# Optimization experiments

Measured on AMD Instinct MI355X. Metric: run time of the kernel, lower is better.

Reference implementation:

```python
import jax, jax.numpy as jnp
import numpy as np
from jax import lax

B, L, D = 8, 2048, 512


def _mlp(x, w1, w2):
    # MemoryMLP: x + gelu(x @ w1) @ w2  (exact gelu, matching F.gelu default)
    return x + jax.nn.gelu(x @ w1, approximate=False) @ w2


def _l2norm(t):
    # F.normalize(p=2, dim=-1, eps=1e-12)
    n = jnp.linalg.norm(t, axis=-1, keepdims=True)
    return t / jnp.maximum(n, 1e-12)


def setup_inputs() -> dict:
    key = jax.random.key(0)
    ks = jax.random.split(key, 12)
    s = 0.02
    return {
        "x": jax.random.normal(ks[0], (B, L, D), jnp.float32),
        "conv_w": jax.random.normal(ks[1], (D, 1, 4), jnp.float32) * s,  # depthwise, (out, in/groups, k)
        "conv_b": jax.random.normal(ks[2], (D,), jnp.float32) * s,
        "q_w": jax.random.normal(ks[3], (D, D), jnp.float32) * s,  # Linear weight (out, in)
        "mem_w1": jax.random.normal(ks[4], (D, D), jnp.float32) * s,
        "mem_w2": jax.random.normal(ks[5], (D, D), jnp.float32) * s,
        "eta_w1": jax.random.normal(ks[6], (D, D), jnp.float32) * s,
        "eta_w2": jax.random.normal(ks[7], (D, D), jnp.float32) * s,
        "alpha_w1": jax.random.normal(ks[8], (D, D), jnp.float32) * s,
        "alpha_w2": jax.random.normal(ks[9], (D, D), jnp.float32) * s,
    }


def _forward(x, conv_w, conv_b, q_w, mem_w1, mem_w2, eta_w1, eta_w2, alpha_w1, alpha_w2):
    # causal depthwise conv: Conv1d(k=4, padding=3, groups=D) then slice [:L] == left-pad 3
    xc = lax.conv_general_dilated(
        jnp.transpose(x, (0, 2, 1)),  # (B, D, L)
        conv_w,                        # (D, 1, 4)
        window_strides=(1,),
        padding=[(3, 0)],
        feature_group_count=D,
        dimension_numbers=("NCH", "OIH", "NCH"),
    ) + conv_b[None, :, None]
    xc = jnp.transpose(xc, (0, 2, 1))  # (B, L, D)

    # time-invariant branches (m_k/m_v weights are never updated; kt/vt/hat_v do not
    # affect the output, so they are elided). q, eta, alpha use fixed weights -> vectorize.
    q = _l2norm(xc @ q_w.T)                                   # (B, L, D)
    eta_mean = jax.nn.sigmoid(_mlp(xc, eta_w1, eta_w2)).mean(axis=(0, 2))      # (L,)
    alpha_mean = jax.nn.sigmoid(_mlp(xc, alpha_w1, alpha_w2)).mean(axis=(0, 2))  # (L,)

    def step(carry, inp):
        w1, w2 = carry
        q_t, a_t, e_t = inp  # (B, D), (), ()
        o_t = _mlp(q_t, w1, w2)  # output uses pre-update memory
        new_w1 = w1 * a_t - e_t * 0.01
        new_w2 = w2 * a_t - e_t * 0.01
        return (new_w1, new_w2), o_t

    qs = jnp.transpose(q, (1, 0, 2))  # (L, B, D)
    (_, _), outs = lax.scan(step, (mem_w1, mem_w2), (qs, alpha_mean, eta_mean))
    return jnp.transpose(outs, (1, 0, 2))  # (B, L, D)


def reference(x, conv_w, conv_b, q_w, mem_w1, mem_w2, eta_w1, eta_w2, alpha_w1, alpha_w2):
    return _forward(x, conv_w, conv_b, q_w, mem_w1, mem_w2, eta_w1, eta_w2, alpha_w1, alpha_w2)
```

## Files before the change

kernel.cpp:

```cpp
#include <hip/hip_runtime.h>
#include <math.h>

constexpr int Bn = 8, Ln = 2048, Dn = 512;
constexpr int Mn = Bn * Ln;
constexpr int CONV_BLOCKS = Mn * Dn / 4 / 256;

typedef __bf16 bf16x8 __attribute__((ext_vector_type(8)));
typedef __bf16 bf16x4v __attribute__((ext_vector_type(4)));
typedef float f32x4 __attribute__((ext_vector_type(4)));

__device__ __forceinline__ float gelu_exact(float x) {
    return 0.5f * x * (1.0f + erff(x * 0.7071067811865475f));
}
__device__ __forceinline__ float sigmoid_fast(float x) {
    return __builtin_amdgcn_rcpf(1.0f + __expf(-x));
}

__global__ __launch_bounds__(256) void prep_kernel(
    const float* __restrict__ x, const float* __restrict__ w,
    const float* __restrict__ bias, __bf16* __restrict__ xcb,
    const float* __restrict__ ew1, const float* __restrict__ aw1,
    const float* __restrict__ ew2, const float* __restrict__ aw2,
    const float* __restrict__ mw1, const float* __restrict__ mw2,
    const float* __restrict__ qw,
    __bf16* __restrict__ Wall, __bf16* __restrict__ W2t,
    __bf16* __restrict__ m1t, __bf16* __restrict__ m2t) {
    __shared__ float tile[64][65];
    if (blockIdx.x < CONV_BLOCKS) {
        int idx = blockIdx.x * 256 + threadIdx.x;
        int g = idx & 127;
        int bl = idx >> 7;
        int l = bl & (Ln - 1);
        int d = g * 4;
        float a[4];
        float4 b4 = *(const float4*)&bias[d];
        a[0] = b4.x; a[1] = b4.y; a[2] = b4.z; a[3] = b4.w;
        float wv[16];
        *(float4*)&wv[0]  = *(const float4*)&w[d * 4];
        *(float4*)&wv[4]  = *(const float4*)&w[d * 4 + 4];
        *(float4*)&wv[8]  = *(const float4*)&w[d * 4 + 8];
        *(float4*)&wv[12] = *(const float4*)&w[d * 4 + 12];
#pragma unroll
        for (int k = 0; k < 4; ++k) {
            int ll = l - 3 + k;
            if (ll >= 0) {
                float4 xv = *(const float4*)&x[(size_t)(bl - 3 + k) * Dn + d];
                a[0] += xv.x * wv[0 * 4 + k];
                a[1] += xv.y * wv[1 * 4 + k];
                a[2] += xv.z * wv[2 * 4 + k];
                a[3] += xv.w * wv[3 * 4 + k];
            }
        }
        bf16x4v o = { (__bf16)a[0], (__bf16)a[1], (__bf16)a[2], (__bf16)a[3] };
        *(bf16x4v*)&xcb[(size_t)bl * Dn + d] = o;
        return;
    }
    int bid = blockIdx.x - CONV_BLOCKS;
    int z = bid >> 6;
    int t = bid & 63;
    int r0 = (t >> 3) * 64, c0 = (t & 7) * 64;
    const float* src;
    __bf16* dst;
    int trans = 1;
    switch (z) {
        case 0: src = ew1; dst = Wall; break;
        case 1: src = aw1; dst = Wall + 512 * 512; break;
        case 2: src = ew2; dst = W2t; break;
        case 3: src = aw2; dst = W2t + 512 * 512; break;
        case 4: src = mw1; dst = m1t; break;
        case 5: src = mw2; dst = m2t; break;
        default: src = qw; dst = Wall + 1024 * 512; trans = 0; break;
    }
    if (!trans) {
        for (int i = threadIdx.x; i < 4096; i += 256) {
            int r = i >> 6, c = i & 63;
            dst[(size_t)(r0 + r) * 512 + c0 + c] = (__bf16)src[(size_t)(r0 + r) * 512 + c0 + c];
        }
        return;
    }
    for (int i = threadIdx.x; i < 4096; i += 256) {
        int r = i >> 6, c = i & 63;
        tile[r][c] = src[(size_t)(r0 + r) * 512 + c0 + c];
    }
    __syncthreads();
    for (int i = threadIdx.x; i < 4096; i += 256) {
        int r = i >> 6, c = i & 63;
        dst[(size_t)(c0 + r) * 512 + r0 + c] = (__bf16)tile[c][r];
    }
}

template <int OP, int BM>
__global__ __launch_bounds__(256, 2) void gemm_mfma(
    const __bf16* __restrict__ A, int lda, int Az,
    const __bf16* __restrict__ Bt, int Bz,
    void* __restrict__ C0, void* __restrict__ C1,
    const __bf16* __restrict__ auxb,
    const float* __restrict__ Pv, const float* __restrict__ Qv,
    const float* __restrict__ SSv, const float* __restrict__ RSv,
    float* __restrict__ red0, float* __restrict__ red1, float* __restrict__ red2) {
    constexpr int MI = BM / 32;
    constexpr int AISS = BM / 64;
    __shared__ __align__(16) __bf16 Asl[BM * 32];
    __shared__ __align__(16) __bf16 Bsl[128 * 32];
    const int tid = threadIdx.x;
    const int lane = tid & 63, wv = tid >> 6;
    const int wm = wv & 1, wn = wv >> 1;
    const int fr = lane & 15, fq = lane >> 4;
    const int z = blockIdx.z;
    A += (size_t)z * Az;
    Bt += (size_t)z * Bz;
    const __bf16* Ab = A + (size_t)blockIdx.y * BM * lda;
    const __bf16* Bb = Bt + (size_t)blockIdx.x * 128 * 512;
    float* redp = (OP == 1) ? red0 + (size_t)z * Ln : red0;

    f32x4 acc[MI][4] = {};

    for (int k0 = 0; k0 < 512; k0 += 32) {
#pragma unroll
        for (int i = 0; i < AISS; ++i) {
            int c = tid + i * 256;
            int r = c >> 2, co = (c & 3) * 8;
            __builtin_amdgcn_global_load_lds(
                (const __attribute__((address_space(1))) void*)(Ab + (size_t)r * lda + k0 + co),
                (__attribute__((address_space(3))) void*)(Asl + c * 8), 16, 0, 0);
        }
#pragma unroll
        for (int i = 0; i < 2; ++i) {
            int c = tid + i * 256;
            int r = c >> 2, co = (c & 3) * 8;
            __builtin_amdgcn_global_load_lds(
                (const __attribute__((address_space(1))) void*)(Bb + (size_t)r * 512 + k0 + co),
                (__attribute__((address_space(3))) void*)(Bsl + c * 8), 16, 0, 0);
        }
        __syncthreads();
        bf16x8 af[MI], bfr[4];
#pragma unroll
        for (int mi = 0; mi < MI; ++mi)
            af[mi] = *(const bf16x8*)&Asl[(wm * (BM / 2) + mi * 16 + fr) * 32 + fq * 8];
#pragma unroll
        for (int ni = 0; ni < 4; ++ni)
            bfr[ni] = *(const bf16x8*)&Bsl[(wn * 64 + ni * 16 + fr) * 32 + fq * 8];
#pragma unroll
        for (int mi = 0; mi < MI; ++mi)
#pragma unroll
            for (int ni = 0; ni < 4; ++ni)
                acc[mi][ni] = __builtin_amdgcn_mfma_f32_16x16x32_bf16(af[mi], bfr[ni], acc[mi][ni], 0, 0, 0);
        __syncthreads();
    }

    const int row_base = blockIdx.y * BM + wm * (BM / 2);
    const int col_base = blockIdx.x * 128 + wn * 64;
    const bool qpath = (OP == 0) && (blockIdx.x >= 8);
#pragma unroll
    for (int mi = 0; mi < MI; ++mi) {
#pragma unroll
        for (int r = 0; r < 4; ++r) {
            int row = row_base + mi * 16 + fq * 4 + r;
            float p = 0.f, qs = 0.f, rs = 0.f, inv = 1.f;
            if (OP >= 3) {
                int t = row & (Ln - 1);
                p = Pv[t]; qs = Qv[t];
                rs = RSv[row];
                inv = 1.0f / fmaxf(sqrtf(SSv[row]), 1e-12f);
            }
            float s1 = 0.f, s2 = 0.f;
#pragma unroll
            for (int ni = 0; ni < 4; ++ni) {
                int col = col_base + ni * 16 + fr;
                float v = acc[mi][ni][r];
                if (OP == 0) {
                    if (!qpath) {
                        v = gelu_exact(v);
                        ((__bf16*)C0)[(size_t)row * 1024 + col] = (__bf16)v;
                    } else {
                        ((__bf16*)C1)[(size_t)row * 512 + col - 1024] = (__bf16)v;
                        s1 += v; s2 += v * v;
                    }
                } else if (OP == 1) {
                    v = sigmoid_fast((float)auxb[(size_t)row * 512 + col] + v);
                    s1 += v;
                } else if (OP == 3) {
                    v = gelu_exact(inv * (p * v + qs * rs));
                    ((__bf16*)C0)[(size_t)row * 512 + col] = (__bf16)v;
                    s1 += v;
                } else if (OP == 4) {
                    float qn = (float)auxb[(size_t)row * 512 + col] * inv;
                    ((float*)C0)[(size_t)row * 512 + col] = qn + p * v + qs * rs;
                }
            }
            if (OP == 1 || OP == 3 || (OP == 0 && qpath)) {
                s1 += __shfl_xor(s1, 1, 64);
                s1 += __shfl_xor(s1, 2, 64);
                s1 += __shfl_xor(s1, 4, 64);
                s1 += __shfl_xor(s1, 8, 64);
                if (OP == 0) {
                    s2 += __shfl_xor(s2, 1, 64);
                    s2 += __shfl_xor(s2, 2, 64);
                    s2 += __shfl_xor(s2, 4, 64);
                    s2 += __shfl_xor(s2, 8, 64);
                }
                if (fr == 0) {
                    if (OP == 1) atomicAdd(&redp[row & (Ln - 1)], s1 * (1.0f / 4096.0f));
                    else if (OP == 3) atomicAdd(&red0[row], s1);
                    else { atomicAdd(&red1[row], s2); atomicAdd(&red2[row], s1); }
                }
            }
        }
    }
}

__global__ __launch_bounds__(256) void scan_kernel(const float* __restrict__ a,
                                                   const float* __restrict__ e,
                                                   float* __restrict__ P,
                                                   float* __restrict__ Q) {
    int tid = threadIdx.x;
    int base = tid * 8;
    float la[8], le[8], Aloc[8], Bloc[8];
#pragma unroll
    for (int j = 0; j < 8; ++j) { la[j] = a[base + j]; le[j] = e[base + j]; }
    float Ac = 1.f, Bc = 0.f;
#pragma unroll
    for (int j = 0; j < 8; ++j) {
        Aloc[j] = Ac; Bloc[j] = Bc;
        Bc = Bc * la[j] - 0.01f * le[j];
        Ac *= la[j];
    }
    float Aw = Ac, Bw = Bc;
#pragma unroll
    for (int off = 1; off < 64; off <<= 1) {
        float Ap = __shfl_up(Aw, off, 64);
        float Bp = __shfl_up(Bw, off, 64);
        if ((tid & 63) >= off) { Bw = Aw * Bp + Bw; Aw = Aw * Ap; }
    }
    __shared__ float wA[4], wB[4];
    if ((tid & 63) == 63) { wA[tid >> 6] = Aw; wB[tid >> 6] = Bw; }
    __syncthreads();
    float Apre = 1.f, Bpre = 0.f;
    for (int w = 0; w < (tid >> 6); ++w) { Bpre = wA[w] * Bpre + wB[w]; Apre = wA[w] * Apre; }
    float Ax = __shfl_up(Aw, 1, 64), Bx = __shfl_up(Bw, 1, 64);
    if ((tid & 63) == 0) { Ax = 1.f; Bx = 0.f; }
    float At = Ax * Apre, Bt2 = Ax * Bpre + Bx;
#pragma unroll
    for (int j = 0; j < 8; ++j) {
        P[base + j] = Aloc[j] * At;
        Q[base + j] = Aloc[j] * Bt2 + Bloc[j];
    }
}

extern "C" void kernel_launch(void* const* d_in, const int* in_sizes, int n_in,
                              void* d_out, int out_size, void* d_ws, size_t ws_size,
                              hipStream_t stream) {
    const float* x        = (const float*)d_in[0];
    const float* conv_w   = (const float*)d_in[1];
    const float* conv_b   = (const float*)d_in[2];
    const float* q_w      = (const float*)d_in[3];
    const float* mem_w1   = (const float*)d_in[4];
    const float* mem_w2   = (const float*)d_in[5];
    const float* eta_w1   = (const float*)d_in[6];
    const float* eta_w2   = (const float*)d_in[7];
    const float* alpha_w1 = (const float*)d_in[8];
    const float* alpha_w2 = (const float*)d_in[9];
    float* out = (float*)d_out;

    char* w = (char*)d_ws;
    __bf16* xcb  = (__bf16*)w;    w += (size_t)Mn * Dn * 2;
    __bf16* H    = (__bf16*)w;    w += (size_t)Mn * 1024 * 2;
    __bf16* qb   = (__bf16*)w;    w += (size_t)Mn * Dn * 2;
    __bf16* G    = (__bf16*)w;    w += (size_t)Mn * Dn * 2;
    __bf16* Wall = (__bf16*)w;    w += (size_t)1536 * 512 * 2;
    __bf16* W2t  = (__bf16*)w;    w += (size_t)2 * 512 * 512 * 2;
    __bf16* m1t  = (__bf16*)w;    w += (size_t)512 * 512 * 2;
    __bf16* m2t  = (__bf16*)w;    w += (size_t)512 * 512 * 2;
    float* Rv      = (float*)w;   w += (size_t)Mn * 4;
    float* MeanAcc = (float*)w;   w += (size_t)2 * Ln * 4;
    float* SS      = (float*)w;   w += (size_t)Mn * 4;
    float* RS      = (float*)w;   w += (size_t)Mn * 4;
    float* Pv = (float*)w;        w += Ln * 4;
    float* Qv = (float*)w;        w += Ln * 4;

    hipMemsetAsync(Rv, 0, (size_t)(Mn + 2 * Ln + Mn + Mn) * 4, stream);

    prep_kernel<<<CONV_BLOCKS + 448, 256, 0, stream>>>(
        x, conv_w, conv_b, xcb, eta_w1, alpha_w1, eta_w2, alpha_w2,
        mem_w1, mem_w2, q_w, Wall, W2t, m1t, m2t);
    gemm_mfma<0, 128><<<dim3(12, 128), 256, 0, stream>>>(
        xcb, 512, 0, Wall, 0, H, qb, nullptr,
        nullptr, nullptr, nullptr, nullptr, nullptr, SS, RS);
    gemm_mfma<1, 128><<<dim3(4, 128, 2), 256, 0, stream>>>(
        H, 1024, 512, W2t, 512 * 512, nullptr, nullptr, xcb,
        nullptr, nullptr, nullptr, nullptr, MeanAcc, nullptr, nullptr);
    scan_kernel<<<1, 256, 0, stream>>>(MeanAcc + Ln, MeanAcc, Pv, Qv);
    gemm_mfma<3, 64><<<dim3(4, 256), 256, 0, stream>>>(
        qb, 512, 0, m1t, 0, G, nullptr, nullptr,
        Pv, Qv, SS, RS, Rv, nullptr, nullptr);
    gemm_mfma<4, 64><<<dim3(4, 256), 256, 0, stream>>>(
        G, 512, 0, m2t, 0, out, nullptr, qb,
        Pv, Qv, SS, Rv, nullptr, nullptr, nullptr);
}
```

Measured before the change: 263.0 us.

## Fuse workspace zeroing into prep kernel and compute four conv rows per thread

Replaces the separate memset with extra zeroing blocks in the prep kernel, removing one launch. The depthwise conv now computes four consecutive rows per thread from seven loaded input rows, so input loads are reused across outputs. The GEMM launch bounds now ask for four blocks per CU, which caps registers per thread and risks spills in exchange for higher occupancy.

New measurement: 245.6 us. -6.6%, faster.

```diff
diff --git a/kernel.cpp b/kernel.cpp
--- a/kernel.cpp
+++ b/kernel.cpp
@@ -3,7 +3,10 @@
 
 constexpr int Bn = 8, Ln = 2048, Dn = 512;
 constexpr int Mn = Bn * Ln;
-constexpr int CONV_BLOCKS = Mn * Dn / 4 / 256;
+constexpr int CONV_BLOCKS = Mn * Dn / 16 / 256;
+constexpr int WPREP_BLOCKS = 448;
+constexpr int ZERO_FLOATS = 3 * Mn + 2 * Ln;
+constexpr int ZERO_BLOCKS = ZERO_FLOATS / (256 * 4);
 
 typedef __bf16 bf16x8 __attribute__((ext_vector_type(8)));
 typedef __bf16 bf16x4v __attribute__((ext_vector_type(4)));
@@ -24,35 +27,51 @@
     const float* __restrict__ mw1, const float* __restrict__ mw2,
     const float* __restrict__ qw,
     __bf16* __restrict__ Wall, __bf16* __restrict__ W2t,
-    __bf16* __restrict__ m1t, __bf16* __restrict__ m2t) {
+    __bf16* __restrict__ m1t, __bf16* __restrict__ m2t,
+    float* __restrict__ zero_zone) {
     __shared__ float tile[64][65];
     if (blockIdx.x < CONV_BLOCKS) {
         int idx = blockIdx.x * 256 + threadIdx.x;
         int g = idx & 127;
-        int bl = idx >> 7;
-        int l = bl & (Ln - 1);
+        int r4 = idx >> 7;
+        int bl0 = r4 * 4;
+        int l0 = bl0 & (Ln - 1);
         int d = g * 4;
-        float a[4];
         float4 b4 = *(const float4*)&bias[d];
-        a[0] = b4.x; a[1] = b4.y; a[2] = b4.z; a[3] = b4.w;
         float wv[16];
         *(float4*)&wv[0]  = *(const float4*)&w[d * 4];
         *(float4*)&wv[4]  = *(const float4*)&w[d * 4 + 4];
         *(float4*)&wv[8]  = *(const float4*)&w[d * 4 + 8];
         *(float4*)&wv[12] = *(const float4*)&w[d * 4 + 12];
-#pragma unroll
-        for (int k = 0; k < 4; ++k) {
-            int ll = l - 3 + k;
-            if (ll >= 0) {
-                float4 xv = *(const float4*)&x[(size_t)(bl - 3 + k) * Dn + d];
-                a[0] += xv.x * wv[0 * 4 + k];
-                a[1] += xv.y * wv[1 * 4 + k];
-                a[2] += xv.z * wv[2 * 4 + k];
-                a[3] += xv.w * wv[3 * 4 + k];
-            }
-        }
-        bf16x4v o = { (__bf16)a[0], (__bf16)a[1], (__bf16)a[2], (__bf16)a[3] };
-        *(bf16x4v*)&xcb[(size_t)bl * Dn + d] = o;
+        float4 xv[7];
+#pragma unroll
+        for (int t = 0; t < 7; ++t) {
+            int ll = l0 - 3 + t;
+            xv[t] = (ll >= 0 && t < 7) ? *(const float4*)&x[(size_t)(bl0 - 3 + t) * Dn + d]
+                                       : make_float4(0.f, 0.f, 0.f, 0.f);
+            if (t >= 3) {
+                if (l0 - 3 + t < Ln) xv[t] = *(const float4*)&x[(size_t)(bl0 - 3 + t) * Dn + d];
+            }
+        }
+#pragma unroll
+        for (int i = 0; i < 4; ++i) {
+            float a0 = b4.x, a1 = b4.y, a2 = b4.z, a3 = b4.w;
+#pragma unroll
+            for (int k = 0; k < 4; ++k) {
+                float4 xt = xv[i + k];
+                a0 += xt.x * wv[0 * 4 + k];
+                a1 += xt.y * wv[1 * 4 + k];
+                a2 += xt.z * wv[2 * 4 + k];
+                a3 += xt.w * wv[3 * 4 + k];
+            }
+            bf16x4v o = { (__bf16)a0, (__bf16)a1, (__bf16)a2, (__bf16)a3 };
+            *(bf16x4v*)&xcb[(size_t)(bl0 + i) * Dn + d] = o;
+        }
+        return;
+    }
+    if (blockIdx.x >= CONV_BLOCKS + WPREP_BLOCKS) {
+        int idx = (blockIdx.x - CONV_BLOCKS - WPREP_BLOCKS) * 256 + threadIdx.x;
+        ((float4*)zero_zone)[idx] = make_float4(0.f, 0.f, 0.f, 0.f);
         return;
     }
     int bid = blockIdx.x - CONV_BLOCKS;
@@ -90,7 +109,7 @@
 }
 
 template <int OP, int BM>
-__global__ __launch_bounds__(256, 2) void gemm_mfma(
+__global__ __launch_bounds__(256, 4) void gemm_mfma(
     const __bf16* __restrict__ A, int lda, int Az,
     const __bf16* __restrict__ Bt, int Bz,
     void* __restrict__ C0, void* __restrict__ C1,
@@ -278,11 +297,9 @@
     float* Pv = (float*)w;        w += Ln * 4;
     float* Qv = (float*)w;        w += Ln * 4;
 
-    hipMemsetAsync(Rv, 0, (size_t)(Mn + 2 * Ln + Mn + Mn) * 4, stream);
-
-    prep_kernel<<<CONV_BLOCKS + 448, 256, 0, stream>>>(
+    prep_kernel<<<CONV_BLOCKS + WPREP_BLOCKS + ZERO_BLOCKS, 256, 0, stream>>>(
         x, conv_w, conv_b, xcb, eta_w1, alpha_w1, eta_w2, alpha_w2,
-        mem_w1, mem_w2, q_w, Wall, W2t, m1t, m2t);
+        mem_w1, mem_w2, q_w, Wall, W2t, m1t, m2t, Rv);
     gemm_mfma<0, 128><<<dim3(12, 128), 256, 0, stream>>>(
         xcb, 512, 0, Wall, 0, H, qb, nullptr,
         nullptr, nullptr, nullptr, nullptr, nullptr, SS, RS);
```
